# Kernel optimization log

Measured on AMD Instinct MI355X. Metric: run time of the kernel, lower is better.

## Reference

```python
import jax, jax.numpy as jnp
import numpy as np

B_, N, C, H = 2048, 49, 384, 12
WH, WW = 7, 7
HEAD_DIM = C // H
SCALE = HEAD_DIM ** -0.5
TABLE = (2 * WH - 1) * (2 * WW - 1)  # 169


def _relative_position_index():
    coords = np.stack(np.meshgrid(np.arange(WH), np.arange(WW), indexing='ij'))  # [2,Wh,Ww]
    flat = coords.reshape(2, -1)  # [2,N]
    rel = flat[:, :, None] - flat[:, None, :]  # [2,N,N]
    rel = rel.transpose(1, 2, 0).astype(np.int32)  # [N,N,2]
    rel[:, :, 0] += WH - 1
    rel[:, :, 1] += WW - 1
    rel[:, :, 0] *= 2 * WW - 1
    return rel.sum(-1)  # [N,N] int32 in [0,169)


def setup_inputs() -> dict:
    key = jax.random.key(0)
    ks = jax.random.split(key, 8)
    return {
        'x': jax.random.normal(ks[0], (B_, N, C), jnp.float32),
        'mask': jax.random.normal(ks[1], (B_, 1, N, N), jnp.float32),
        'stagein': jax.random.uniform(ks[2], (B_, N, C), jnp.float32),
        'rel_bias_table': jax.random.normal(ks[3], (TABLE, H), jnp.float32) * 0.02,
        'rel_pos_index': jnp.asarray(_relative_position_index()),
        'qkv_w': jax.random.normal(ks[4], (3 * C, C), jnp.float32) * 0.02,
        'qkv_b': jax.random.normal(ks[5], (3 * C,), jnp.float32) * 0.02,
        'proj_w': jax.random.normal(ks[6], (C, C), jnp.float32) * 0.02,
        'proj_b': jax.random.normal(ks[7], (C,), jnp.float32) * 0.02,
    }


def reference(x, mask, stagein, rel_bias_table, rel_pos_index, qkv_w, qkv_b, proj_w, proj_b):
    x = x * stagein  # stagein is not None branch
    qkv = x @ qkv_w.T + qkv_b  # [B_, N, 3C]
    qkv = qkv.reshape(B_, N, 3, H, HEAD_DIM).transpose(2, 0, 3, 1, 4)  # [3,B_,H,N,hd]
    q, k, v = qkv[0], qkv[1], qkv[2]
    q = q * SCALE
    attn = jnp.einsum('bhnd,bhmd->bhnm', q, k)  # [B_,H,N,N]
    # relative position bias gather: [N*N] -> [N,N,H] -> [1,H,N,N]
    bias = rel_bias_table[rel_pos_index.reshape(-1)].reshape(N, N, H)
    bias = bias.transpose(2, 0, 1)[None]
    attn = jax.nn.softmax(attn + bias + mask, axis=-1)
    out = jnp.einsum('bhnm,bhmd->bhnd', attn, v)  # [B_,H,N,hd]
    out = out.transpose(0, 2, 1, 3).reshape(B_, N, C)
    return out @ proj_w.T + proj_b
```

## Files before the change

### kernel.cpp

```cpp
#include <hip/hip_runtime.h>
#include <hip/hip_bf16.h>
#include <stdint.h>

#define NWIN 2048
#define NTOK 49
#define CDIM 384
#define NHEAD 12
#define HD 32
#define C3 1152
#define NN2 2401
#define MROWS 100352

typedef __bf16 bf16x8 __attribute__((ext_vector_type(8)));
typedef float f32x4 __attribute__((ext_vector_type(4)));
typedef uint32_t u32x4 __attribute__((ext_vector_type(4)));

static __device__ __forceinline__ unsigned short f2bf(float f) {
  uint32_t u = __builtin_bit_cast(uint32_t, f);
  u += 0x7fffu + ((u >> 16) & 1u);
  return (unsigned short)(u >> 16);
}

static __device__ __forceinline__ void gload_lds16(const void* g, void* l) {
  __builtin_amdgcn_global_load_lds((const __attribute__((address_space(1))) void*)g,
                                   (__attribute__((address_space(3))) void*)l,
                                   16, 0, 0);
}

static __device__ __forceinline__ bf16x8 zero8() {
  u32x4 z = {0u, 0u, 0u, 0u};
  return __builtin_bit_cast(bf16x8, z);
}

__global__ void prep_kernel(const float* __restrict__ qkv_w, const float* __restrict__ proj_w,
                            const float* __restrict__ table, const int* __restrict__ idx,
                            unsigned short* __restrict__ wq, unsigned short* __restrict__ wp,
                            float* __restrict__ biasexp) {
  const int NW1 = C3 * CDIM;
  const int NW2 = CDIM * CDIM;
  const int NB = NHEAD * NN2;
  int i = blockIdx.x * blockDim.x + threadIdx.x;
  int stride = gridDim.x * blockDim.x;
  for (int t = i; t < NW1 + NW2 + NB; t += stride) {
    if (t < NW1) {
      wq[t] = f2bf(qkv_w[t]);
    } else if (t < NW1 + NW2) {
      int j = t - NW1;
      wp[j] = f2bf(proj_w[j]);
    } else {
      int j = t - NW1 - NW2;
      int h = j / NN2;
      int nm = j - h * NN2;
      biasexp[j] = table[idx[nm] * NHEAD + h];
    }
  }
}

__global__ void mul_kernel(const float4* __restrict__ x, const float4* __restrict__ s,
                           u32x4* __restrict__ A, int n8) {
  int i0 = blockIdx.x * blockDim.x + threadIdx.x;
  int stride = gridDim.x * blockDim.x;
  for (int t = i0; t < n8; t += stride) {
    float4 a0 = x[2 * t], a1 = x[2 * t + 1];
    float4 b0 = s[2 * t], b1 = s[2 * t + 1];
    union { unsigned short us[8]; u32x4 v; } o;
    o.us[0] = f2bf(a0.x * b0.x); o.us[1] = f2bf(a0.y * b0.y);
    o.us[2] = f2bf(a0.z * b0.z); o.us[3] = f2bf(a0.w * b0.w);
    o.us[4] = f2bf(a1.x * b1.x); o.us[5] = f2bf(a1.y * b1.y);
    o.us[6] = f2bf(a1.z * b1.z); o.us[7] = f2bf(a1.w * b1.w);
    A[t] = o.v;
  }
}

__launch_bounds__(256, 2)
__global__ void qkv_gemm(const unsigned short* __restrict__ A,
                         const unsigned short* __restrict__ Bw,
                         const float* __restrict__ qkvb,
                         unsigned short* __restrict__ qo,
                         unsigned short* __restrict__ ko,
                         unsigned short* __restrict__ vo) {
  __shared__ unsigned short As[128 * 32];
  __shared__ unsigned short Bs[128 * 32];
  const int tid = threadIdx.x;
  const int w = tid >> 6, l = tid & 63;
  const int l15 = l & 15, lhi = l >> 4;
  const int mt = blockIdx.x / 9, nt = blockIdx.x - mt * 9;
  const int wr = w >> 1, wc = w & 1;
  const int srow = w * 32 + (l >> 2);
  const int skk = (l & 3) * 8;
  const unsigned short* Ag = A + (size_t)(mt * 128 + srow) * CDIM + skk;
  const unsigned short* Bg = Bw + (size_t)(nt * 128 + srow) * CDIM + skk;
  unsigned short* Asl = As + (w * 1024 + l * 8);
  unsigned short* Bsl = Bs + (w * 1024 + l * 8);
  const f32x4 z4 = {0.f, 0.f, 0.f, 0.f};
  f32x4 acc[4][4];
#pragma unroll
  for (int m = 0; m < 4; ++m)
#pragma unroll
    for (int n = 0; n < 4; ++n) acc[m][n] = z4;
  for (int kt = 0; kt < 12; ++kt) {
    const unsigned short* ag = Ag + kt * 32;
    const unsigned short* bg = Bg + kt * 32;
    gload_lds16(ag, Asl);
    gload_lds16(ag + 16 * CDIM, Asl + 512);
    gload_lds16(bg, Bsl);
    gload_lds16(bg + 16 * CDIM, Bsl + 512);
    __syncthreads();
    bf16x8 af[4], bfr[4];
#pragma unroll
    for (int m = 0; m < 4; ++m)
      af[m] = *(const bf16x8*)(As + (wr * 64 + m * 16 + l15) * 32 + lhi * 8);
#pragma unroll
    for (int n = 0; n < 4; ++n)
      bfr[n] = *(const bf16x8*)(Bs + (wc * 64 + n * 16 + l15) * 32 + lhi * 8);
#pragma unroll
    for (int m = 0; m < 4; ++m)
#pragma unroll
      for (int n = 0; n < 4; ++n)
        acc[m][n] = __builtin_amdgcn_mfma_f32_16x16x32_bf16(af[m], bfr[n], acc[m][n], 0, 0, 0);
    __syncthreads();
  }
  const int six = nt * 2 + wc;
  const int which = six / 6;
  const int cbase = (six - which * 6) * 64;
  unsigned short* outw = (which == 0) ? qo : ((which == 1) ? ko : vo);
  const float* bptr = qkvb + which * CDIM;
#pragma unroll
  for (int m = 0; m < 4; ++m) {
#pragma unroll
    for (int j = 0; j < 4; ++j) {
      const int r = mt * 128 + wr * 64 + m * 16 + lhi * 4 + j;
      const int bwin = r / 49;
      const int ntok = r - bwin * 49;
#pragma unroll
      for (int n = 0; n < 4; ++n) {
        const int c = cbase + n * 16 + l15;
        const int h = c >> 5, d = c & 31;
        const float val = acc[m][n][j] + bptr[c];
        outw[(((size_t)bwin * NHEAD + h) * NTOK + ntok) * HD + d] = f2bf(val);
      }
    }
  }
}

__launch_bounds__(256, 2)
__global__ void attn_kernel(const unsigned short* __restrict__ q,
                            const unsigned short* __restrict__ kmat,
                            const unsigned short* __restrict__ vmat,
                            const float* __restrict__ mask,
                            const float* __restrict__ biasexp,
                            unsigned short* __restrict__ attnout) {
  __shared__ unsigned short P_lds[4][64 * 72];
  __shared__ unsigned short vT_lds[4][32 * 72];
  const int tid = threadIdx.x;
  const int w = tid >> 6, l = tid & 63;
  const int l15 = l & 15, lhi = l >> 4;
  const int b = blockIdx.x;
  unsigned short* Pw = &P_lds[w][0];
  unsigned short* Vw = &vT_lds[w][0];
  const float* maskb = mask + (size_t)b * NN2;
  const float SCALE = 0.17677669529663687f;
  const f32x4 z4 = {0.f, 0.f, 0.f, 0.f};
  for (int it = 0; it < 3; ++it) {
    const int h = it * 4 + w;
    const size_t hb = ((size_t)b * NHEAD + h) * NTOK * HD;
    const unsigned short* qb = q + hb;
    const unsigned short* kb = kmat + hb;
    const unsigned short* vb = vmat + hb;
    {
      const int n = l;
      unsigned short tmp[32];
      if (n < 49) {
        *(u32x4*)(&tmp[0])  = *(const u32x4*)(vb + n * 32);
        *(u32x4*)(&tmp[8])  = *(const u32x4*)(vb + n * 32 + 8);
        *(u32x4*)(&tmp[16]) = *(const u32x4*)(vb + n * 32 + 16);
        *(u32x4*)(&tmp[24]) = *(const u32x4*)(vb + n * 32 + 24);
      } else {
#pragma unroll
        for (int d2 = 0; d2 < 32; ++d2) tmp[d2] = 0;
      }
#pragma unroll
      for (int d2 = 0; d2 < 32; ++d2) Vw[d2 * 72 + n] = tmp[d2];
    }
    bf16x8 aq[4], bk[4];
#pragma unroll
    for (int t = 0; t < 4; ++t) {
      const int row = t * 16 + l15;
      if (row < 49) {
        aq[t] = *(const bf16x8*)(qb + row * 32 + lhi * 8);
        bk[t] = *(const bf16x8*)(kb + row * 32 + lhi * 8);
      } else {
        aq[t] = zero8();
        bk[t] = zero8();
      }
    }
    f32x4 s[4][4];
#pragma unroll
    for (int ti = 0; ti < 4; ++ti)
#pragma unroll
      for (int tj = 0; tj < 4; ++tj)
        s[ti][tj] = __builtin_amdgcn_mfma_f32_16x16x32_bf16(aq[ti], bk[tj], z4, 0, 0, 0);
    const float* biash = biasexp + h * NN2;
#pragma unroll
    for (int ti = 0; ti < 4; ++ti) {
#pragma unroll
      for (int r = 0; r < 4; ++r) {
        const int n = ti * 16 + lhi * 4 + r;
#pragma unroll
        for (int tj = 0; tj < 4; ++tj) {
          const int m = tj * 16 + l15;
          float val = -1e30f;
          if (n < 49 && m < 49)
            val = s[ti][tj][r] * SCALE + biash[n * 49 + m] + maskb[n * 49 + m];
          s[ti][tj][r] = val;
        }
      }
    }
#pragma unroll
    for (int ti = 0; ti < 4; ++ti) {
#pragma unroll
      for (int r = 0; r < 4; ++r) {
        float mx = fmaxf(fmaxf(s[ti][0][r], s[ti][1][r]), fmaxf(s[ti][2][r], s[ti][3][r]));
        mx = fmaxf(mx, __shfl_xor(mx, 1));
        mx = fmaxf(mx, __shfl_xor(mx, 2));
        mx = fmaxf(mx, __shfl_xor(mx, 4));
        mx = fmaxf(mx, __shfl_xor(mx, 8));
        float e0 = __expf(s[ti][0][r] - mx);
        float e1 = __expf(s[ti][1][r] - mx);
        float e2 = __expf(s[ti][2][r] - mx);
        float e3 = __expf(s[ti][3][r] - mx);
        float sum = (e0 + e1) + (e2 + e3);
        sum += __shfl_xor(sum, 1);
        sum += __shfl_xor(sum, 2);
        sum += __shfl_xor(sum, 4);
        sum += __shfl_xor(sum, 8);
        const float rinv = 1.0f / sum;
        const int n = ti * 16 + lhi * 4 + r;
        unsigned short* pr = Pw + n * 72 + l15;
        pr[0]  = f2bf(e0 * rinv);
        pr[16] = f2bf(e1 * rinv);
        pr[32] = f2bf(e2 * rinv);
        pr[48] = f2bf(e3 * rinv);
      }
    }
    f32x4 o[4][2];
#pragma unroll
    for (int ti = 0; ti < 4; ++ti) { o[ti][0] = z4; o[ti][1] = z4; }
#pragma unroll
    for (int kk = 0; kk < 2; ++kk) {
      bf16x8 pa[4], bv[2];
#pragma unroll
      for (int ti = 0; ti < 4; ++ti)
        pa[ti] = *(const bf16x8*)(Pw + (ti * 16 + l15) * 72 + kk * 32 + lhi * 8);
#pragma unroll
      for (int dj = 0; dj < 2; ++dj)
        bv[dj] = *(const bf16x8*)(Vw + (dj * 16 + l15) * 72 + kk * 32 + lhi * 8);
#pragma unroll
      for (int ti = 0; ti < 4; ++ti)
#pragma unroll
        for (int dj = 0; dj < 2; ++dj)
          o[ti][dj] = __builtin_amdgcn_mfma_f32_16x16x32_bf16(pa[ti], bv[dj], o[ti][dj], 0, 0, 0);
    }
#pragma unroll
    for (int ti = 0; ti < 4; ++ti) {
#pragma unroll
      for (int r = 0; r < 4; ++r) {
        const int n = ti * 16 + lhi * 4 + r;
        if (n < 49) {
          unsigned short* orow = attnout + ((size_t)b * NTOK + n) * CDIM + h * HD;
          orow[l15] = f2bf(o[ti][0][r]);
          orow[16 + l15] = f2bf(o[ti][1][r]);
        }
      }
    }
  }
}

__launch_bounds__(256, 2)
__global__ void proj_gemm(const unsigned short* __restrict__ A,
                          const unsigned short* __restrict__ Bw,
                          const float* __restrict__ pb,
                          float* __restrict__ out) {
  __shared__ unsigned short As[128 * 32];
  __shared__ unsigned short Bs[128 * 32];
  const int tid = threadIdx.x;
  const int w = tid >> 6, l = tid & 63;
  const int l15 = l & 15, lhi = l >> 4;
  const int mt = blockIdx.x / 3, nt = blockIdx.x - mt * 3;
  const int wr = w >> 1, wc = w & 1;
  const int srow = w * 32 + (l >> 2);
  const int skk = (l & 3) * 8;
  const unsigned short* Ag = A + (size_t)(mt * 128 + srow) * CDIM + skk;
  const unsigned short* Bg = Bw + (size_t)(nt * 128 + srow) * CDIM + skk;
  unsigned short* Asl = As + (w * 1024 + l * 8);
  unsigned short* Bsl = Bs + (w * 1024 + l * 8);
  const f32x4 z4 = {0.f, 0.f, 0.f, 0.f};
  f32x4 acc[4][4];
#pragma unroll
  for (int m = 0; m < 4; ++m)
#pragma unroll
    for (int n = 0; n < 4; ++n) acc[m][n] = z4;
  for (int kt = 0; kt < 12; ++kt) {
    const unsigned short* ag = Ag + kt * 32;
    const unsigned short* bg = Bg + kt * 32;
    gload_lds16(ag, Asl);
    gload_lds16(ag + 16 * CDIM, Asl + 512);
    gload_lds16(bg, Bsl);
    gload_lds16(bg + 16 * CDIM, Bsl + 512);
    __syncthreads();
    bf16x8 af[4], bfr[4];
#pragma unroll
    for (int m = 0; m < 4; ++m)
      af[m] = *(const bf16x8*)(As + (wr * 64 + m * 16 + l15) * 32 + lhi * 8);
#pragma unroll
    for (int n = 0; n < 4; ++n)
      bfr[n] = *(const bf16x8*)(Bs + (wc * 64 + n * 16 + l15) * 32 + lhi * 8);
#pragma unroll
    for (int m = 0; m < 4; ++m)
#pragma unroll
      for (int n = 0; n < 4; ++n)
        acc[m][n] = __builtin_amdgcn_mfma_f32_16x16x32_bf16(af[m], bfr[n], acc[m][n], 0, 0, 0);
    __syncthreads();
  }
#pragma unroll
  for (int m = 0; m < 4; ++m) {
#pragma unroll
    for (int j = 0; j < 4; ++j) {
      const int r = mt * 128 + wr * 64 + m * 16 + lhi * 4 + j;
      float* orow = out + (size_t)r * CDIM;
#pragma unroll
      for (int n = 0; n < 4; ++n) {
        const int c = nt * 128 + wc * 64 + n * 16 + l15;
        orow[c] = acc[m][n][j] + pb[c];
      }
    }
  }
}

extern "C" void kernel_launch(void* const* d_in, const int* in_sizes, int n_in,
                              void* d_out, int out_size, void* d_ws, size_t ws_size,
                              hipStream_t stream) {
  const float* x       = (const float*)d_in[0];
  const float* mask    = (const float*)d_in[1];
  const float* stagein = (const float*)d_in[2];
  const float* table   = (const float*)d_in[3];
  const int*   idx     = (const int*)d_in[4];
  const float* qkv_w   = (const float*)d_in[5];
  const float* qkv_b   = (const float*)d_in[6];
  const float* proj_w  = (const float*)d_in[7];
  const float* proj_b  = (const float*)d_in[8];
  float* out = (float*)d_out;
  char* ws = (char*)d_ws;

  const size_t SZA = (size_t)MROWS * CDIM * 2;
  unsigned short* Abf = (unsigned short*)(ws);
  unsigned short* qb  = (unsigned short*)(ws + SZA);
  unsigned short* kb  = (unsigned short*)(ws + 2 * SZA);
  unsigned short* vb  = (unsigned short*)(ws + 3 * SZA);
  unsigned short* wq  = (unsigned short*)(ws + 4 * SZA);
  unsigned short* wp  = (unsigned short*)(ws + 4 * SZA + (size_t)C3 * CDIM * 2);
  float* biasexp      = (float*)(ws + 4 * SZA + (size_t)C3 * CDIM * 2 + (size_t)CDIM * CDIM * 2);
  unsigned short* attnout = Abf;

  prep_kernel<<<dim3(512), dim3(256), 0, stream>>>(qkv_w, proj_w, table, idx, wq, wp, biasexp);
  mul_kernel<<<dim3(2048), dim3(256), 0, stream>>>((const float4*)x, (const float4*)stagein,
                                                   (u32x4*)Abf, MROWS * CDIM / 8);
  qkv_gemm<<<dim3(784 * 9), dim3(256), 0, stream>>>(Abf, wq, qkv_b, qb, kb, vb);
  attn_kernel<<<dim3(NWIN), dim3(256), 0, stream>>>(qb, kb, vb, mask, biasexp, attnout);
  proj_gemm<<<dim3(784 * 3), dim3(256), 0, stream>>>(attnout, wp, proj_b, out);
}
```

Baseline: 458.2 us.

## Deepen GEMM K-tiles to 64 with XOR-swizzled LDS, remap blocks, fold scale

Both GEMMs now stage 64-wide K slices (6 iterations instead of 12) with an XOR swizzle on the LDS column blocks, which is meant to halve barrier count and avoid bank conflicts on the fragment reads. Blocks are remapped in an 8-way interleave, likely to spread them across XCDs or improve L2 locality. Occupancy hints go from 2 to 4 blocks per CU. The softmax scale moves into the QKV epilogue so the attention kernel skips one multiply per score, which slightly changes bf16 rounding of q.

```diff
diff --git a/kernel.cpp b/kernel.cpp
--- a/kernel.cpp
+++ b/kernel.cpp
@@ -72,54 +72,62 @@
   }
 }
 
-__launch_bounds__(256, 2)
+__launch_bounds__(256, 4)
 __global__ void qkv_gemm(const unsigned short* __restrict__ A,
                          const unsigned short* __restrict__ Bw,
                          const float* __restrict__ qkvb,
                          unsigned short* __restrict__ qo,
                          unsigned short* __restrict__ ko,
                          unsigned short* __restrict__ vo) {
-  __shared__ unsigned short As[128 * 32];
-  __shared__ unsigned short Bs[128 * 32];
+  __shared__ unsigned short As[128 * 64];
+  __shared__ unsigned short Bs[128 * 64];
   const int tid = threadIdx.x;
   const int w = tid >> 6, l = tid & 63;
   const int l15 = l & 15, lhi = l >> 4;
-  const int mt = blockIdx.x / 9, nt = blockIdx.x - mt * 9;
+  const int wgid = (blockIdx.x & 7) * 882 + (blockIdx.x >> 3);
+  const int mt = wgid / 9, nt = wgid - mt * 9;
   const int wr = w >> 1, wc = w & 1;
-  const int srow = w * 32 + (l >> 2);
-  const int skk = (l & 3) * 8;
-  const unsigned short* Ag = A + (size_t)(mt * 128 + srow) * CDIM + skk;
-  const unsigned short* Bg = Bw + (size_t)(nt * 128 + srow) * CDIM + skk;
-  unsigned short* Asl = As + (w * 1024 + l * 8);
-  unsigned short* Bsl = Bs + (w * 1024 + l * 8);
+  const int srow = tid >> 3;
+  const int scb = (tid & 7) ^ (srow & 7);
+  const unsigned short* Ag = A + (size_t)(mt * 128 + srow) * CDIM + scb * 8;
+  const unsigned short* Bg = Bw + (size_t)(nt * 128 + srow) * CDIM + scb * 8;
+  unsigned short* Asl = As + srow * 64 + (tid & 7) * 8;
+  unsigned short* Bsl = Bs + srow * 64 + (tid & 7) * 8;
   const f32x4 z4 = {0.f, 0.f, 0.f, 0.f};
   f32x4 acc[4][4];
 #pragma unroll
   for (int m = 0; m < 4; ++m)
 #pragma unroll
     for (int n = 0; n < 4; ++n) acc[m][n] = z4;
-  for (int kt = 0; kt < 12; ++kt) {
-    const unsigned short* ag = Ag + kt * 32;
-    const unsigned short* bg = Bg + kt * 32;
-    gload_lds16(ag, Asl);
-    gload_lds16(ag + 16 * CDIM, Asl + 512);
-    gload_lds16(bg, Bsl);
-    gload_lds16(bg + 16 * CDIM, Bsl + 512);
+  const int xr = l15 & 7;
+  for (int kt = 0; kt < 6; ++kt) {
+    const unsigned short* ag = Ag + kt * 64;
+    const unsigned short* bg = Bg + kt * 64;
+#pragma unroll
+    for (int i = 0; i < 4; ++i) {
+      gload_lds16(ag + i * 32 * CDIM, Asl + i * 2048);
+      gload_lds16(bg + i * 32 * CDIM, Bsl + i * 2048);
+    }
     __syncthreads();
-    bf16x8 af[4], bfr[4];
-#pragma unroll
-    for (int m = 0; m < 4; ++m)
-      af[m] = *(const bf16x8*)(As + (wr * 64 + m * 16 + l15) * 32 + lhi * 8);
-#pragma unroll
-    for (int n = 0; n < 4; ++n)
-      bfr[n] = *(const bf16x8*)(Bs + (wc * 64 + n * 16 + l15) * 32 + lhi * 8);
-#pragma unroll
-    for (int m = 0; m < 4; ++m)
+#pragma unroll
+    for (int kk = 0; kk < 2; ++kk) {
+      const int sl = ((kk << 2) | lhi) ^ xr;
+      bf16x8 af[4], bfr[4];
+#pragma unroll
+      for (int m = 0; m < 4; ++m)
+        af[m] = *(const bf16x8*)(As + (wr * 64 + m * 16 + l15) * 64 + sl * 8);
 #pragma unroll
       for (int n = 0; n < 4; ++n)
-        acc[m][n] = __builtin_amdgcn_mfma_f32_16x16x32_bf16(af[m], bfr[n], acc[m][n], 0, 0, 0);
+        bfr[n] = *(const bf16x8*)(Bs + (wc * 64 + n * 16 + l15) * 64 + sl * 8);
+#pragma unroll
+      for (int m = 0; m < 4; ++m)
+#pragma unroll
+        for (int n = 0; n < 4; ++n)
+          acc[m][n] = __builtin_amdgcn_mfma_f32_16x16x32_bf16(af[m], bfr[n], acc[m][n], 0, 0, 0);
+    }
     __syncthreads();
   }
+  const float SCALE_F = 0.17677669529663687f;
   const int six = nt * 2 + wc;
   const int which = six / 6;
   const int cbase = (six - which * 6) * 64;
@@ -136,7 +144,8 @@
       for (int n = 0; n < 4; ++n) {
         const int c = cbase + n * 16 + l15;
         const int h = c >> 5, d = c & 31;
-        const float val = acc[m][n][j] + bptr[c];
+        float val = acc[m][n][j] + bptr[c];
+        if (which == 0) val *= SCALE_F;
         outw[(((size_t)bwin * NHEAD + h) * NTOK + ntok) * HD + d] = f2bf(val);
       }
     }
@@ -159,7 +168,6 @@
   unsigned short* Pw = &P_lds[w][0];
   unsigned short* Vw = &vT_lds[w][0];
   const float* maskb = mask + (size_t)b * NN2;
-  const float SCALE = 0.17677669529663687f;
   const f32x4 z4 = {0.f, 0.f, 0.f, 0.f};
   for (int it = 0; it < 3; ++it) {
     const int h = it * 4 + w;
@@ -211,7 +219,7 @@
           const int m = tj * 16 + l15;
           float val = -1e30f;
           if (n < 49 && m < 49)
-            val = s[ti][tj][r] * SCALE + biash[n * 49 + m] + maskb[n * 49 + m];
+            val = s[ti][tj][r] + biash[n * 49 + m] + maskb[n * 49 + m];
           s[ti][tj][r] = val;
         }
       }
@@ -276,50 +284,57 @@
   }
 }
 
-__launch_bounds__(256, 2)
+__launch_bounds__(256, 4)
 __global__ void proj_gemm(const unsigned short* __restrict__ A,
                           const unsigned short* __restrict__ Bw,
                           const float* __restrict__ pb,
                           float* __restrict__ out) {
-  __shared__ unsigned short As[128 * 32];
-  __shared__ unsigned short Bs[128 * 32];
+  __shared__ unsigned short As[128 * 64];
+  __shared__ unsigned short Bs[128 * 64];
   const int tid = threadIdx.x;
   const int w = tid >> 6, l = tid & 63;
   const int l15 = l & 15, lhi = l >> 4;
-  const int mt = blockIdx.x / 3, nt = blockIdx.x - mt * 3;
+  const int wgid = (blockIdx.x & 7) * 294 + (blockIdx.x >> 3);
+  const int mt = wgid / 3, nt = wgid - mt * 3;
   const int wr = w >> 1, wc = w & 1;
-  const int srow = w * 32 + (l >> 2);
-  const int skk = (l & 3) * 8;
-  const unsigned short* Ag = A + (size_t)(mt * 128 + srow) * CDIM + skk;
-  const unsigned short* Bg = Bw + (size_t)(nt * 128 + srow) * CDIM + skk;
-  unsigned short* Asl = As + (w * 1024 + l * 8);
-  unsigned short* Bsl = Bs + (w * 1024 + l * 8);
+  const int srow = tid >> 3;
+  const int scb = (tid & 7) ^ (srow & 7);
+  const unsigned short* Ag = A + (size_t)(mt * 128 + srow) * CDIM + scb * 8;
+  const unsigned short* Bg = Bw + (size_t)(nt * 128 + srow) * CDIM + scb * 8;
+  unsigned short* Asl = As + srow * 64 + (tid & 7) * 8;
+  unsigned short* Bsl = Bs + srow * 64 + (tid & 7) * 8;
   const f32x4 z4 = {0.f, 0.f, 0.f, 0.f};
   f32x4 acc[4][4];
 #pragma unroll
   for (int m = 0; m < 4; ++m)
 #pragma unroll
     for (int n = 0; n < 4; ++n) acc[m][n] = z4;
-  for (int kt = 0; kt < 12; ++kt) {
-    const unsigned short* ag = Ag + kt * 32;
-    const unsigned short* bg = Bg + kt * 32;
-    gload_lds16(ag, Asl);
-    gload_lds16(ag + 16 * CDIM, Asl + 512);
-    gload_lds16(bg, Bsl);
-    gload_lds16(bg + 16 * CDIM, Bsl + 512);
+  const int xr = l15 & 7;
+  for (int kt = 0; kt < 6; ++kt) {
+    const unsigned short* ag = Ag + kt * 64;
+    const unsigned short* bg = Bg + kt * 64;
+#pragma unroll
+    for (int i = 0; i < 4; ++i) {
+      gload_lds16(ag + i * 32 * CDIM, Asl + i * 2048);
+      gload_lds16(bg + i * 32 * CDIM, Bsl + i * 2048);
+    }
     __syncthreads();
-    bf16x8 af[4], bfr[4];
-#pragma unroll
-    for (int m = 0; m < 4; ++m)
-      af[m] = *(const bf16x8*)(As + (wr * 64 + m * 16 + l15) * 32 + lhi * 8);
-#pragma unroll
-    for (int n = 0; n < 4; ++n)
-      bfr[n] = *(const bf16x8*)(Bs + (wc * 64 + n * 16 + l15) * 32 + lhi * 8);
-#pragma unroll
-    for (int m = 0; m < 4; ++m)
+#pragma unroll
+    for (int kk = 0; kk < 2; ++kk) {
+      const int sl = ((kk << 2) | lhi) ^ xr;
+      bf16x8 af[4], bfr[4];
+#pragma unroll
+      for (int m = 0; m < 4; ++m)
+        af[m] = *(const bf16x8*)(As + (wr * 64 + m * 16 + l15) * 64 + sl * 8);
 #pragma unroll
       for (int n = 0; n < 4; ++n)
-        acc[m][n] = __builtin_amdgcn_mfma_f32_16x16x32_bf16(af[m], bfr[n], acc[m][n], 0, 0, 0);
+        bfr[n] = *(const bf16x8*)(Bs + (wc * 64 + n * 16 + l15) * 64 + sl * 8);
+#pragma unroll
+      for (int m = 0; m < 4; ++m)
+#pragma unroll
+        for (int n = 0; n < 4; ++n)
+          acc[m][n] = __builtin_amdgcn_mfma_f32_16x16x32_bf16(af[m], bfr[n], acc[m][n], 0, 0, 0);
+    }
     __syncthreads();
   }
 #pragma unroll
```

After: 518.7 us. 13.2% more time.
